# Optimization experiments

Measured on AMD Instinct MI355X. Metric: run time of the kernel, lower is better.

## Reference

```python
import jax, jax.numpy as jnp
import numpy as np

N = 100000   # nodes
E = 1600000  # directed edges
F_IN, F_HID, F_OUT = 10, 64, 4


def setup_inputs() -> dict:
    key = jax.random.key(0)
    ks = jax.random.split(key, 8)
    x = jax.random.normal(ks[0], (N, F_IN), dtype=jnp.float32)
    edge_index = jax.random.randint(ks[1], (2, E), 0, N, dtype=jnp.int64)
    W1 = jax.random.normal(ks[2], (F_IN, F_HID), dtype=jnp.float32) * (1.0 / np.sqrt(F_IN))
    b1 = jnp.zeros((F_HID,), dtype=jnp.float32)
    W2 = jax.random.normal(ks[3], (F_HID, F_HID), dtype=jnp.float32) * (1.0 / np.sqrt(F_HID))
    b2 = jnp.zeros((F_HID,), dtype=jnp.float32)
    W3 = jax.random.normal(ks[4], (F_HID, F_OUT), dtype=jnp.float32) * (1.0 / np.sqrt(F_HID))
    b3 = jnp.zeros((F_OUT,), dtype=jnp.float32)
    return {"x": x, "edge_index": edge_index, "W1": W1, "b1": b1,
            "W2": W2, "b2": b2, "W3": W3, "b3": b3}


def _gcn_layer(h_in, W, b, src, dst, dinv_sqrt):
    # GCNConv: D^{-1/2} (A + I) D^{-1/2} (h_in W) + b, with deg counted incl. self-loops
    h = h_in @ W                                   # [N, F_out]
    norm = dinv_sqrt[src] * dinv_sqrt[dst]         # [E]
    msg = h[src] * norm[:, None]                   # [E, F_out]  (dominant traffic)
    agg = jax.ops.segment_sum(msg, dst, num_segments=N)
    agg = agg + h * (dinv_sqrt * dinv_sqrt)[:, None]  # self-loop contribution
    return agg + b


def reference(x, edge_index, W1, b1, W2, b2, W3, b3):
    src, dst = edge_index[0], edge_index[1]
    # degree of target nodes including self-loop
    deg = jax.ops.segment_sum(jnp.ones((E,), x.dtype), dst, num_segments=N) + 1.0
    dinv_sqrt = jax.lax.rsqrt(deg)
    h = jax.nn.relu(_gcn_layer(x, W1, b1, src, dst, dinv_sqrt))
    # dropout is identity in eval mode (training=False)
    h = jax.nn.relu(_gcn_layer(h, W2, b2, src, dst, dinv_sqrt))
    h = _gcn_layer(h, W3, b3, src, dst, dinv_sqrt)
    return jax.nn.log_softmax(h, axis=1)
```

## Files before the change

kernel.cpp:

```cpp
#include <hip/hip_runtime.h>
#include <hip/hip_bf16.h>
#include <math.h>


#define D_MAX 48
#define BUCK_SH 7
#define NPB 128
#define NBK 782
#define P1_BLOCKS 256
#define P1_THREADS 512
#define SEG_CAP 36

typedef __hip_bfloat16 bf16;
typedef int int4v __attribute__((ext_vector_type(4)));

__global__ void k_bin(const int* __restrict__ src, const int* __restrict__ dst,
                      int* __restrict__ arena, int* __restrict__ cnt2, int E) {
    __shared__ int lcnt[NBK];
    int t = threadIdx.x, blk = blockIdx.x;
    for (int i = t; i < NBK; i += P1_THREADS) lcnt[i] = 0;
    __syncthreads();
#define BIN_ONE(d_, s_) {                                                     \
        int b_ = (d_) >> BUCK_SH;                                             \
        int rec_ = ((d_) & (NPB - 1)) | ((s_) << BUCK_SH);                    \
        int slot_ = atomicAdd(&lcnt[b_], 1);                                  \
        if (slot_ < SEG_CAP)                                                  \
            arena[(size_t)b_ * (P1_BLOCKS * SEG_CAP) + slot_ * P1_BLOCKS + blk] = rec_; \
    }
    int E4 = E >> 2;
    int chunk4 = (E4 + P1_BLOCKS - 1) / P1_BLOCKS;
    int q0 = blk * chunk4;
    int q1 = min(q0 + chunk4, E4);
    for (int q = q0 + t; q < q1; q += P1_THREADS) {
        int4v d4 = __builtin_nontemporal_load((const int4v*)dst + q);
        int4v s4 = __builtin_nontemporal_load((const int4v*)src + q);
        BIN_ONE(d4.x, s4.x);
        BIN_ONE(d4.y, s4.y);
        BIN_ONE(d4.z, s4.z);
        BIN_ONE(d4.w, s4.w);
    }
    if (blk == 0 && t < (E & 3)) {
        int e = (E & ~3) + t;
        BIN_ONE(dst[e], src[e]);
    }
#undef BIN_ONE
    __syncthreads();
    for (int b = t; b < NBK; b += P1_THREADS)
        cnt2[b * P1_BLOCKS + blk] = lcnt[b];
}

__global__ void k_ellbuild(const int* __restrict__ arena, const int* __restrict__ cnt2,
                           const float* __restrict__ x,
                           int* __restrict__ ell, int* __restrict__ cnt,
                           float* __restrict__ dinv, bf16* __restrict__ xp, int N) {
    __shared__ int cnt128[NPB];
    __shared__ int ellb[NPB * D_MAX];
    __shared__ float dloc[NPB];
    int t = threadIdx.x, b = blockIdx.x;
    if (t < NPB) cnt128[t] = 0;
    __syncthreads();
    int cc = min(cnt2[b * P1_BLOCKS + t], SEG_CAP);
    const int* base = arena + (size_t)b * (P1_BLOCKS * SEG_CAP);
    for (int i = 0; i < SEG_CAP; ++i) {
        if (i < cc) {
            int rec = base[i * P1_BLOCKS + t];
            int r = rec & (NPB - 1);
            int s = rec >> BUCK_SH;
            int slot = atomicAdd(&cnt128[r], 1);
            if (slot < D_MAX) ellb[r * D_MAX + slot] = s;
        }
        if (__builtin_amdgcn_ballot_w64(i + 1 < cc) == 0) break;
    }
    __syncthreads();
    int nb = b << BUCK_SH;
    if (t < NPB) {
        int n = nb + t;
        if (n < N) {
            int dg = cnt128[t];
            cnt[n] = dg;
            float dv = rsqrtf((float)dg + 1.0f);
            dinv[n] = dv;
            dloc[t] = dv;
        }
    }
    __syncthreads();
    const int ROWQ = D_MAX / 4;
    for (int i4 = t; i4 < NPB * ROWQ; i4 += 256) {
        int n = nb + i4 / ROWQ;
        if (n < N)
            ((int4v*)(ell + (size_t)nb * D_MAX))[i4] = ((const int4v*)ellb)[i4];
    }
    for (int i = t; i < NPB * 10; i += 256) {
        int n = nb + i / 10;
        if (n < N) xp[(size_t)nb * 10 + i] = __float2bfloat16(x[(size_t)nb * 10 + i] * dloc[i / 10]);
    }
}

__global__ void k_gather10(const int* __restrict__ ell, const int* __restrict__ cnt,
                           const bf16* __restrict__ xp, const float* __restrict__ dinv,
                           float* __restrict__ aggx, int N) {
    int tid = threadIdx.x;
    int g = tid & 15;
    int node = blockIdx.x * 16 + (tid >> 4);
    if (node >= N) return;
    int deg = cnt[node]; if (deg > D_MAX) deg = D_MAX;
    float acc = 0.0f;
    for (int c0 = 0; c0 < deg; c0 += 16) {
        int m = deg - c0; if (m > 16) m = 16;
        int sid = 0;
        if (g < m) sid = ell[(size_t)node * D_MAX + c0 + g];
        for (int i = 0; i < m; ++i) {
            int s = __shfl(sid, i, 16);
            if (g < 10) acc += __bfloat162float(xp[(size_t)s * 10 + g]);
        }
    }
    if (g < 10) {
        acc += __bfloat162float(xp[(size_t)node * 10 + g]);
        aggx[(size_t)node * 10 + g] = dinv[node] * acc;
    }
}

__global__ void k_fused1(const float* __restrict__ aggx, const float* __restrict__ W1,
                         const float* __restrict__ b1, const float* __restrict__ W2,
                         const float* __restrict__ dinv, bf16* __restrict__ t, int N) {
    __shared__ float W1s[10 * 64];
    __shared__ float h1s[64][64];
    int tid = threadIdx.x;
    int f = tid & 63, w = tid >> 6;
    float w2c[64];
#pragma unroll
    for (int k = 0; k < 64; ++k) w2c[k] = W2[k * 64 + f];
    for (int i = tid; i < 640; i += 256) W1s[i] = W1[i];
    __syncthreads();
    int nb = blockIdx.x * 64;
    float bf = b1[f];
    for (int j = 0; j < 16; ++j) {
        int ln = w * 16 + j;
        int n = nb + ln;
        float acc = bf;
        if (n < N) {
#pragma unroll
            for (int k = 0; k < 10; ++k)
                acc = fmaf(aggx[(size_t)n * 10 + k], W1s[k * 64 + f], acc);
        }
        h1s[ln][f] = fmaxf(acc, 0.0f);
    }
    __syncthreads();
    for (int j = 0; j < 16; ++j) {
        int ln = w * 16 + j;
        int n = nb + ln;
        if (n >= N) continue;
        float acc = 0.0f;
        const float4* hr = (const float4*)h1s[ln];
#pragma unroll
        for (int k4 = 0; k4 < 16; ++k4) {
            float4 h = hr[k4];
            acc = fmaf(h.x, w2c[k4 * 4 + 0], acc);
            acc = fmaf(h.y, w2c[k4 * 4 + 1], acc);
            acc = fmaf(h.z, w2c[k4 * 4 + 2], acc);
            acc = fmaf(h.w, w2c[k4 * 4 + 3], acc);
        }
        t[(size_t)n * 64 + f] = __float2bfloat16(acc * dinv[n]);
    }
}

__global__ void k_fused2(const int* __restrict__ ell, const int* __restrict__ cnt,
                         const bf16* __restrict__ t, const float* __restrict__ dinv,
                         const float* __restrict__ b2, const float* __restrict__ W3,
                         float* __restrict__ t3, int N) {
    __shared__ float W3s[256];
    int tid = threadIdx.x;
    W3s[tid] = W3[tid];
    __syncthreads();
    int f = tid & 63;
    int node = blockIdx.x * 4 + (tid >> 6);
    if (node >= N) return;
    int deg = cnt[node]; if (deg > D_MAX) deg = D_MAX;
    int sid = 0;
    if (f < deg) sid = ell[(size_t)node * D_MAX + f];
    float acc = 0.0f;
    int i = 0;
    for (; i + 8 <= deg; i += 8) {
        int s0 = __shfl(sid, i),     s1 = __shfl(sid, i + 1);
        int s2 = __shfl(sid, i + 2), s3 = __shfl(sid, i + 3);
        int s4 = __shfl(sid, i + 4), s5 = __shfl(sid, i + 5);
        int s6 = __shfl(sid, i + 6), s7 = __shfl(sid, i + 7);
        float v0 = __bfloat162float(t[(size_t)s0 * 64 + f]);
        float v1 = __bfloat162float(t[(size_t)s1 * 64 + f]);
        float v2 = __bfloat162float(t[(size_t)s2 * 64 + f]);
        float v3 = __bfloat162float(t[(size_t)s3 * 64 + f]);
        float v4 = __bfloat162float(t[(size_t)s4 * 64 + f]);
        float v5 = __bfloat162float(t[(size_t)s5 * 64 + f]);
        float v6 = __bfloat162float(t[(size_t)s6 * 64 + f]);
        float v7 = __bfloat162float(t[(size_t)s7 * 64 + f]);
        acc += ((v0 + v1) + (v2 + v3)) + ((v4 + v5) + (v6 + v7));
    }
    for (; i < deg; ++i) {
        int s = __shfl(sid, i);
        acc += __bfloat162float(t[(size_t)s * 64 + f]);
    }
    float di = dinv[node];
    acc += __bfloat162float(t[(size_t)node * 64 + f]);
    float h2 = fmaxf(di * acc + b2[f], 0.0f);
    float p0 = h2 * W3s[f * 4 + 0];
    float p1 = h2 * W3s[f * 4 + 1];
    float p2 = h2 * W3s[f * 4 + 2];
    float p3 = h2 * W3s[f * 4 + 3];
#pragma unroll
    for (int off = 32; off > 0; off >>= 1) {
        p0 += __shfl_down(p0, off);
        p1 += __shfl_down(p1, off);
        p2 += __shfl_down(p2, off);
        p3 += __shfl_down(p3, off);
    }
    if (f == 0) {
        float4 r = {p0 * di, p1 * di, p2 * di, p3 * di};
        *(float4*)(t3 + (size_t)node * 4) = r;
    }
}

__global__ void k_out(const int* __restrict__ ell, const int* __restrict__ cnt,
                      const float* __restrict__ t3, const float* __restrict__ dinv,
                      const float* __restrict__ b3, float* __restrict__ out, int N) {
    int n = blockIdx.x * blockDim.x + threadIdx.x;
    if (n >= N) return;
    int deg = cnt[n]; if (deg > D_MAX) deg = D_MAX;
    float a0 = 0.f, a1 = 0.f, a2 = 0.f, a3 = 0.f;
    const int* row = ell + (size_t)n * D_MAX;
    for (int c = 0; c < deg; c += 4) {
        int4 q = *(const int4*)(row + c);
        {
            float4 v = *(const float4*)(t3 + (size_t)q.x * 4);
            a0 += v.x; a1 += v.y; a2 += v.z; a3 += v.w;
        }
        if (c + 1 < deg) {
            float4 v = *(const float4*)(t3 + (size_t)q.y * 4);
            a0 += v.x; a1 += v.y; a2 += v.z; a3 += v.w;
        }
        if (c + 2 < deg) {
            float4 v = *(const float4*)(t3 + (size_t)q.z * 4);
            a0 += v.x; a1 += v.y; a2 += v.z; a3 += v.w;
        }
        if (c + 3 < deg) {
            float4 v = *(const float4*)(t3 + (size_t)q.w * 4);
            a0 += v.x; a1 += v.y; a2 += v.z; a3 += v.w;
        }
    }
    float4 sv = *(const float4*)(t3 + (size_t)n * 4);
    a0 += sv.x; a1 += sv.y; a2 += sv.z; a3 += sv.w;
    float di = dinv[n];
    float v0 = di * a0 + b3[0];
    float v1 = di * a1 + b3[1];
    float v2 = di * a2 + b3[2];
    float v3 = di * a3 + b3[3];
    float m = fmaxf(fmaxf(v0, v1), fmaxf(v2, v3));
    float s = expf(v0 - m) + expf(v1 - m) + expf(v2 - m) + expf(v3 - m);
    float ls = m + logf(s);
    float4 r = {v0 - ls, v1 - ls, v2 - ls, v3 - ls};
    *(float4*)(out + (size_t)n * 4) = r;
}

extern "C" void kernel_launch(void* const* d_in, const int* in_sizes, int n_in,
                              void* d_out, int out_size, void* d_ws, size_t ws_size,
                              hipStream_t stream) {
    const float* x  = (const float*)d_in[0];
    const int*   ei = (const int*)d_in[1];
    const float* W1 = (const float*)d_in[2];
    const float* b1 = (const float*)d_in[3];
    const float* W2 = (const float*)d_in[4];
    const float* b2 = (const float*)d_in[5];
    const float* W3 = (const float*)d_in[6];
    const float* b3 = (const float*)d_in[7];
    float* out = (float*)d_out;

    const int E = in_sizes[1] / 2;
    const int N = in_sizes[0] / 10;
    const int* src = ei;
    const int* dst = ei + E;

    float* dinv  = (float*)d_ws;
    int*   cnt   = (int*)(dinv + N);
    int*   ell   = cnt + N;
    bf16*  xp    = (bf16*)(ell + (size_t)N * D_MAX);
    float* t3    = (float*)(xp + (size_t)N * 10 + 8);
    int*   arena = (int*)(t3 + (size_t)N * 4);
    int*   cnt2  = arena + (size_t)NBK * P1_BLOCKS * SEG_CAP;
    float* aggx  = (float*)arena;
    bf16*  tbuf  = (bf16*)(aggx + (size_t)N * 10);

    k_bin<<<P1_BLOCKS, P1_THREADS, 0, stream>>>(src, dst, arena, cnt2, E);
    k_ellbuild<<<NBK, 256, 0, stream>>>(arena, cnt2, x, ell, cnt, dinv, xp, N);

    k_gather10<<<(N + 15) / 16, 256, 0, stream>>>(ell, cnt, xp, dinv, aggx, N);
    k_fused1<<<(N + 63) / 64, 256, 0, stream>>>(aggx, W1, b1, W2, dinv, tbuf, N);
    k_fused2<<<(N + 3) / 4, 256, 0, stream>>>(ell, cnt, tbuf, dinv, b2, W3, t3, N);
    k_out<<<(N + 255) / 256, 256, 0, stream>>>(ell, cnt, t3, dinv, b3, out, N);
}
```

Baseline: 193.9 us.

## Stage binned edges in LDS, write contiguous segments, add overflow list

The binning kernel now buffers each bucket's records in shared memory and writes them out as contiguous vectorized segments per (bucket, block), replacing the scattered strided stores. Bucket size doubles to 256 nodes, so there are half as many buckets, and the ELL build reads segments with int4 loads. Records beyond the per-segment cap now go to a global overflow list instead of being dropped, which the build kernel scans. This adds a memset, a large LDS footprint in k_bin (about 50KB), and a full overflow scan by every build block.

```diff
diff --git a/kernel.cpp b/kernel.cpp
--- a/kernel.cpp
+++ b/kernel.cpp
@@ -4,28 +4,34 @@
 
 
 #define D_MAX 48
-#define BUCK_SH 7
-#define NPB 128
-#define NBK 782
+#define BUCK_SH 8
+#define NPB 256
+#define NBK 391
 #define P1_BLOCKS 256
 #define P1_THREADS 512
-#define SEG_CAP 36
+#define SEG_CAP 32
+#define OFL_CAP 8192
 
 typedef __hip_bfloat16 bf16;
 typedef int int4v __attribute__((ext_vector_type(4)));
 
 __global__ void k_bin(const int* __restrict__ src, const int* __restrict__ dst,
-                      int* __restrict__ arena, int* __restrict__ cnt2, int E) {
+                      int* __restrict__ arena, int* __restrict__ cnt2,
+                      int* __restrict__ ofl_cnt, int2* __restrict__ ofl, int E) {
+    __shared__ int stage[NBK][SEG_CAP];
     __shared__ int lcnt[NBK];
     int t = threadIdx.x, blk = blockIdx.x;
     for (int i = t; i < NBK; i += P1_THREADS) lcnt[i] = 0;
     __syncthreads();
-#define BIN_ONE(d_, s_) {                                                     \
-        int b_ = (d_) >> BUCK_SH;                                             \
-        int rec_ = ((d_) & (NPB - 1)) | ((s_) << BUCK_SH);                    \
-        int slot_ = atomicAdd(&lcnt[b_], 1);                                  \
-        if (slot_ < SEG_CAP)                                                  \
-            arena[(size_t)b_ * (P1_BLOCKS * SEG_CAP) + slot_ * P1_BLOCKS + blk] = rec_; \
+#define BIN_ONE(d_, s_) {                                                   \
+        int b_ = (d_) >> BUCK_SH;                                           \
+        int rec_ = ((d_) & (NPB - 1)) | ((s_) << BUCK_SH);                  \
+        int slot_ = atomicAdd(&lcnt[b_], 1);                                \
+        if (slot_ < SEG_CAP) stage[b_][slot_] = rec_;                       \
+        else {                                                              \
+            int p_ = atomicAdd(ofl_cnt, 1);                                 \
+            if (p_ < OFL_CAP) ofl[p_] = make_int2(b_, rec_);                \
+        }                                                                   \
     }
     int E4 = E >> 2;
     int chunk4 = (E4 + P1_BLOCKS - 1) / P1_BLOCKS;
@@ -47,52 +53,69 @@
     __syncthreads();
     for (int b = t; b < NBK; b += P1_THREADS)
         cnt2[b * P1_BLOCKS + blk] = lcnt[b];
+    for (int i = t; i < NBK * 8; i += P1_THREADS) {
+        int b = i >> 3, q = i & 7;
+        int cc = min(lcnt[b], SEG_CAP);
+        if (q * 4 < cc) {
+            int4v v = ((const int4v*)&stage[b][0])[q];
+            ((int4v*)arena)[((size_t)b * P1_BLOCKS + blk) * (SEG_CAP / 4) + q] = v;
+        }
+    }
 }
 
 __global__ void k_ellbuild(const int* __restrict__ arena, const int* __restrict__ cnt2,
+                           const int* __restrict__ ofl_cnt, const int2* __restrict__ ofl,
                            const float* __restrict__ x,
                            int* __restrict__ ell, int* __restrict__ cnt,
                            float* __restrict__ dinv, bf16* __restrict__ xp, int N) {
-    __shared__ int cnt128[NPB];
     __shared__ int ellb[NPB * D_MAX];
+    __shared__ int cntL[NPB];
     __shared__ float dloc[NPB];
     int t = threadIdx.x, b = blockIdx.x;
-    if (t < NPB) cnt128[t] = 0;
-    __syncthreads();
+    cntL[t] = 0;
+    __syncthreads();
+#define INS_ONE(rec_) {                                                     \
+        int r_ = (rec_) & (NPB - 1);                                        \
+        int s_ = (rec_) >> BUCK_SH;                                         \
+        int slot_ = atomicAdd(&cntL[r_], 1);                                \
+        if (slot_ < D_MAX) ellb[r_ * D_MAX + slot_] = s_;                   \
+    }
     int cc = min(cnt2[b * P1_BLOCKS + t], SEG_CAP);
-    const int* base = arena + (size_t)b * (P1_BLOCKS * SEG_CAP);
-    for (int i = 0; i < SEG_CAP; ++i) {
-        if (i < cc) {
-            int rec = base[i * P1_BLOCKS + t];
-            int r = rec & (NPB - 1);
-            int s = rec >> BUCK_SH;
-            int slot = atomicAdd(&cnt128[r], 1);
-            if (slot < D_MAX) ellb[r * D_MAX + slot] = s;
-        }
-        if (__builtin_amdgcn_ballot_w64(i + 1 < cc) == 0) break;
-    }
+    const int4v* segv = (const int4v*)(arena + ((size_t)b * P1_BLOCKS + t) * SEG_CAP);
+    for (int i4 = 0; i4 * 4 < cc; ++i4) {
+        int4v r4 = segv[i4];
+        int lim = cc - i4 * 4;
+        INS_ONE(r4.x);
+        if (lim > 1) INS_ONE(r4.y);
+        if (lim > 2) INS_ONE(r4.z);
+        if (lim > 3) INS_ONE(r4.w);
+    }
+    int total = min(*ofl_cnt, OFL_CAP);
+    for (int i = t; i < total; i += NPB) {
+        int2 r = ofl[i];
+        if (r.x == b) INS_ONE(r.y);
+    }
+#undef INS_ONE
     __syncthreads();
     int nb = b << BUCK_SH;
-    if (t < NPB) {
-        int n = nb + t;
-        if (n < N) {
-            int dg = cnt128[t];
-            cnt[n] = dg;
-            float dv = rsqrtf((float)dg + 1.0f);
-            dinv[n] = dv;
-            dloc[t] = dv;
-        }
+    int n = nb + t;
+    if (n < N) {
+        int dg = cntL[t];
+        cnt[n] = dg;
+        float dv = rsqrtf((float)dg + 1.0f);
+        dinv[n] = dv;
+        dloc[t] = dv;
     }
     __syncthreads();
     const int ROWQ = D_MAX / 4;
-    for (int i4 = t; i4 < NPB * ROWQ; i4 += 256) {
-        int n = nb + i4 / ROWQ;
-        if (n < N)
+    for (int i4 = t; i4 < NPB * ROWQ; i4 += NPB) {
+        int nn = nb + i4 / ROWQ;
+        if (nn < N)
             ((int4v*)(ell + (size_t)nb * D_MAX))[i4] = ((const int4v*)ellb)[i4];
     }
-    for (int i = t; i < NPB * 10; i += 256) {
-        int n = nb + i / 10;
-        if (n < N) xp[(size_t)nb * 10 + i] = __float2bfloat16(x[(size_t)nb * 10 + i] * dloc[i / 10]);
+    for (int i = t; i < NPB * 10; i += NPB) {
+        int nn = nb + i / 10;
+        if (nn < N) xp[(size_t)nb * 10 + i] = __float2bfloat16(x[(size_t)nb * 10 + i] * dloc[i / 10]);
     }
 }
 
@@ -278,18 +301,21 @@
     const int* src = ei;
     const int* dst = ei + E;
 
-    float* dinv  = (float*)d_ws;
-    int*   cnt   = (int*)(dinv + N);
-    int*   ell   = cnt + N;
-    bf16*  xp    = (bf16*)(ell + (size_t)N * D_MAX);
-    float* t3    = (float*)(xp + (size_t)N * 10 + 8);
-    int*   arena = (int*)(t3 + (size_t)N * 4);
-    int*   cnt2  = arena + (size_t)NBK * P1_BLOCKS * SEG_CAP;
-    float* aggx  = (float*)arena;
-    bf16*  tbuf  = (bf16*)(aggx + (size_t)N * 10);
-
-    k_bin<<<P1_BLOCKS, P1_THREADS, 0, stream>>>(src, dst, arena, cnt2, E);
-    k_ellbuild<<<NBK, 256, 0, stream>>>(arena, cnt2, x, ell, cnt, dinv, xp, N);
+    float* dinv    = (float*)d_ws;
+    int*   cnt     = (int*)(dinv + N);
+    int*   ell     = cnt + N;
+    bf16*  xp      = (bf16*)(ell + (size_t)N * D_MAX);
+    float* t3      = (float*)(xp + (size_t)N * 10 + 8);
+    int*   ofl_cnt = (int*)(t3 + (size_t)N * 4);
+    int2*  ofl     = (int2*)(ofl_cnt + 4);
+    int*   arena   = (int*)(ofl + OFL_CAP);
+    int*   cnt2    = arena + (size_t)NBK * P1_BLOCKS * SEG_CAP;
+    float* aggx    = (float*)arena;
+    bf16*  tbuf    = (bf16*)(aggx + (size_t)N * 10);
+
+    hipMemsetAsync(ofl_cnt, 0, 4 * sizeof(int), stream);
+    k_bin<<<P1_BLOCKS, P1_THREADS, 0, stream>>>(src, dst, arena, cnt2, ofl_cnt, ofl, E);
+    k_ellbuild<<<NBK, NPB, 0, stream>>>(arena, cnt2, ofl_cnt, ofl, x, ell, cnt, dinv, xp, N);
 
     k_gather10<<<(N + 15) / 16, 256, 0, stream>>>(ell, cnt, xp, dinv, aggx, N);
     k_fused1<<<(N + 63) / 64, 256, 0, stream>>>(aggx, W1, b1, W2, dinv, tbuf, N);
```

Result: faster. 172.4 us, median of 2 (-11.1%).
